# Optimization experiments

Measured on AMD Instinct MI355X. Metric: run time of the kernel, lower is better.

## Reference

```python
import jax, jax.numpy as jnp
import numpy as np

EMBED_DIM = 32
PIC_RES = 96
KERNEL_BW = 3.0
STEP_SIZE = 0.5
NB_ITERS = 3


def setup_inputs() -> dict:
    key = jax.random.key(0)
    # scale down so exp(bw * x^T x) stays in a safe numeric range
    x_in = jax.random.normal(key, (1, EMBED_DIM, PIC_RES, PIC_RES), dtype=jnp.float32) * 0.1
    return {"x_in": x_in}


def reference(x_in):
    # x: [D, N], N = res*res pixels
    x = x_in.reshape(EMBED_DIM, -1)
    outs = []
    for _ in range(NB_ITERS):
        # affinity K[i,j] = exp(bw * <x_i, x_j>), shape [N, N]
        K = jnp.exp(KERNEL_BW * (x.T @ x))
        # column sums d_j = sum_i K[i,j] (== torch diag(K^T @ 1)); K is symmetric
        d = K.sum(axis=0)
        # x <- x @ (step * K diag(1/d) + (1-step) I)
        x = STEP_SIZE * (x @ K) / d + (1.0 - STEP_SIZE) * x
        outs.append(x.reshape(EMBED_DIM, PIC_RES, PIC_RES))
    final = x.reshape(EMBED_DIM, PIC_RES, PIC_RES)
    return final, jnp.stack(outs)
```

## Files before the change

### kernel.cpp

```cpp
#include <hip/hip_runtime.h>
#include <hip/hip_bf16.h>
#include <math.h>


#define D 32
#define NPIX 9216
#define NSPLIT 16
#define JB 256
#define NJB (NPIX / JB)
#define IPB (NPIX / NSPLIT)
#define ICH 64
#define XST 56
#define TS  40

typedef __attribute__((ext_vector_type(8))) short short8;
typedef __attribute__((ext_vector_type(4))) short short4v;
typedef __attribute__((ext_vector_type(4))) float f32x4;

#if __has_builtin(__builtin_amdgcn_exp2f)
#define EXP2F __builtin_amdgcn_exp2f
#else
#define EXP2F exp2f
#endif

#define C3 4.32808512266689f

__device__ __forceinline__ unsigned pack2_bf16(float a, float b) {
    union { __hip_bfloat162 h2; unsigned u; } c;
    c.h2 = __float22bfloat162_rn(make_float2(a, b));
    return c.u;
}
__device__ __forceinline__ short pack1_bf16(float a) {
    union { __hip_bfloat16 h; unsigned short s; } c;
    c.h = __float2bfloat16(a);
    return (short)c.s;
}

__global__ __launch_bounds__(256, 2) void accum_kernel(
    const short* __restrict__ xb,
    const short* __restrict__ xbT,
    float* __restrict__ num_part,
    float* __restrict__ den_part)
{
    __shared__ __align__(16) short xiT_s[2][32 * XST];
    __shared__ __align__(16) short xi_s [2][32 * XST];

    const int t = threadIdx.x;
    const int wid = t >> 6, lane = t & 63, quad = lane >> 4, m = lane & 15;
    const int bj = blockIdx.x % NJB, bi = blockIdx.x / NJB;
    const int j0 = bj * JB + wid * 64;
    const int i0b = bi * IPB;

    short8 bfrag[4];
#pragma unroll
    for (int jt = 0; jt < 4; ++jt)
        bfrag[jt] = *(const short8*)&xbT[(size_t)(j0 + jt * 16 + m) * D + quad * 8];

    f32x4 acc[2][4] = {};
    float dacc[4] = {0.f, 0.f, 0.f, 0.f};

    const int srT = t >> 2, hT = srT >> 5, ilT = srT & 31, cT = (t & 3) * 8;
    const int sgm = ((ilT & 4) << 2) + ((ilT >> 3) << 2) + (ilT & 3);
    const int dV = t >> 3, cV = (t & 7) >> 2, qV = (t & 3) * 8;

    for (int ic = 0; ic < IPB; ic += ICH) {
        const int i0 = i0b + ic;
        __syncthreads();
        *(short8*)&xiT_s[hT][sgm * XST + cT] =
            *(const short8*)&xbT[(size_t)(i0 + srT) * D + cT];
        *(short8*)&xi_s[cV][dV * XST + qV] =
            *(const short8*)&xb[dV * NPIX + i0 + cV * 32 + qV];
        __syncthreads();

#pragma unroll
        for (int h = 0; h < 2; ++h) {
            short8 aT0 = *(const short8*)&xiT_s[h][m * XST + quad * 8];
            short8 aT1 = *(const short8*)&xiT_s[h][(16 + m) * XST + quad * 8];
            short8 aV0 = *(const short8*)&xi_s[h][m * XST + quad * 8];
            short8 aV1 = *(const short8*)&xi_s[h][(16 + m) * XST + quad * 8];

#pragma unroll
            for (int jt = 0; jt < 4; ++jt) {
                f32x4 z = {0.f, 0.f, 0.f, 0.f};
                f32x4 s0 = __builtin_amdgcn_mfma_f32_16x16x32_bf16(aT0, bfrag[jt], z, 0, 0, 0);
                f32x4 s1 = __builtin_amdgcn_mfma_f32_16x16x32_bf16(aT1, bfrag[jt], z, 0, 0, 0);

                float w[8];
#pragma unroll
                for (int r = 0; r < 4; ++r) { w[r]     = EXP2F(C3 * s0[r]);
                                              w[4 + r] = EXP2F(C3 * s1[r]); }
#pragma unroll
                for (int r = 0; r < 8; ++r) dacc[jt] += w[r];

                union { short8 s; unsigned u[4]; } wb;
                wb.u[0] = pack2_bf16(w[0], w[1]);
                wb.u[1] = pack2_bf16(w[2], w[3]);
                wb.u[2] = pack2_bf16(w[4], w[5]);
                wb.u[3] = pack2_bf16(w[6], w[7]);

                acc[0][jt] = __builtin_amdgcn_mfma_f32_16x16x32_bf16(aV0, wb.s, acc[0][jt], 0, 0, 0);
                acc[1][jt] = __builtin_amdgcn_mfma_f32_16x16x32_bf16(aV1, wb.s, acc[1][jt], 0, 0, 0);
            }
        }
    }

    float* np = num_part + (size_t)bi * D * NPIX;
#pragma unroll
    for (int dt = 0; dt < 2; ++dt)
#pragma unroll
        for (int jt = 0; jt < 4; ++jt)
#pragma unroll
            for (int r = 0; r < 4; ++r)
                np[(dt * 16 + quad * 4 + r) * NPIX + j0 + jt * 16 + m] = acc[dt][jt][r];
#pragma unroll
    for (int jt = 0; jt < 4; ++jt) {
        float v = dacc[jt];
        v += __shfl_xor(v, 16, 64);
        v += __shfl_xor(v, 32, 64);
        if (quad == 0) den_part[bi * NPIX + j0 + jt * 16 + m] = v;
    }
}

__global__ __launch_bounds__(256) void combine_kernel(
    const float* __restrict__ xin,
    const float* __restrict__ num_part, const float* __restrict__ den_part,
    float* __restrict__ xout, float* __restrict__ xfinal,
    short* __restrict__ xb, short* __restrict__ xbT, int do_ms)
{
    __shared__ __align__(16) short tile[32 * TS];
    const int t = threadIdx.x;
    const int il = t & 31, q = t >> 5;
    const int i = blockIdx.x * 32 + il;
    const int d0 = q * 4;

    float inv = 0.f;
    if (do_ms) {
        float den = 0.f;
#pragma unroll
        for (int s = 0; s < NSPLIT; ++s) den += den_part[s * NPIX + i];
        inv = 0.5f / den;
    }

#pragma unroll
    for (int dd = 0; dd < 4; ++dd) {
        const int d = d0 + dd;
        const int idx = d * NPIX + i;
        float v;
        if (do_ms) {
            float nm = 0.f;
#pragma unroll
            for (int s = 0; s < NSPLIT; ++s) nm += num_part[(s * D + d) * NPIX + i];
            v = nm * inv + 0.5f * xin[idx];
            xout[idx] = v;
            if (xfinal) xfinal[idx] = v;
        } else {
            v = xin[idx];
        }
        short b = pack1_bf16(v);
        xb[idx] = b;
        tile[il * TS + d] = b;
    }
    __syncthreads();
    const int i2 = t >> 3, dc = (t & 7) * 4;
    *(short4v*)&xbT[(blockIdx.x * 32 + i2) * D + dc] =
        *(const short4v*)&tile[i2 * TS + dc];
}

extern "C" void kernel_launch(void* const* d_in, const int* in_sizes, int n_in,
                              void* d_out, int out_size, void* d_ws, size_t ws_size,
                              hipStream_t stream)
{
    const float* x0 = (const float*)d_in[0];
    float* out = (float*)d_out;
    const size_t slot = (size_t)D * NPIX;

    float* num_part = (float*)d_ws;
    float* den_part = num_part + (size_t)NSPLIT * slot;
    short* xb  = (short*)(den_part + (size_t)NSPLIT * NPIX);
    short* xbT = xb + slot;

    combine_kernel<<<dim3(NPIX / 32), dim3(256), 0, stream>>>(
        x0, nullptr, nullptr, nullptr, nullptr, xb, xbT, 0);

    for (int t = 0; t < 3; ++t) {
        accum_kernel<<<dim3(NJB * NSPLIT), dim3(256), 0, stream>>>(
            xb, xbT, num_part, den_part);
        const float* xin = (t == 0) ? x0 : (out + (size_t)t * slot);
        combine_kernel<<<dim3(NPIX / 32), dim3(256), 0, stream>>>(
            xin, num_part, den_part, out + (size_t)(t + 1) * slot,
            (t == 2) ? out : nullptr, xb, xbT, 1);
    }
}
```

Baseline: 173.2 us.

## Accumulate split-K partials with atomics and shrink accum blocks to 128 threads

Replaces the per-split partial numerator and denominator buffers with float atomicAdd into a single accumulator. The combine kernel reads that accumulator directly and zeroes it for the next iteration. The accum kernel now uses 128-thread blocks covering 128 columns, with each thread loading two LDS tiles, which doubles the grid size and targets higher occupancy. This removes the 16-way partial write and readback traffic, at the cost of atomic contention and a floating-point summation order that is no longer deterministic.

```diff
diff --git a/kernel.cpp b/kernel.cpp
--- a/kernel.cpp
+++ b/kernel.cpp
@@ -6,7 +6,7 @@
 #define D 32
 #define NPIX 9216
 #define NSPLIT 16
-#define JB 256
+#define JB 128
 #define NJB (NPIX / JB)
 #define IPB (NPIX / NSPLIT)
 #define ICH 64
@@ -36,11 +36,11 @@
     return (short)c.s;
 }
 
-__global__ __launch_bounds__(256, 2) void accum_kernel(
+__global__ __launch_bounds__(128, 4) void accum_kernel(
     const short* __restrict__ xb,
     const short* __restrict__ xbT,
-    float* __restrict__ num_part,
-    float* __restrict__ den_part)
+    float* __restrict__ num,
+    float* __restrict__ den)
 {
     __shared__ __align__(16) short xiT_s[2][32 * XST];
     __shared__ __align__(16) short xi_s [2][32 * XST];
@@ -59,17 +59,19 @@
     f32x4 acc[2][4] = {};
     float dacc[4] = {0.f, 0.f, 0.f, 0.f};
 
-    const int srT = t >> 2, hT = srT >> 5, ilT = srT & 31, cT = (t & 3) * 8;
-    const int sgm = ((ilT & 4) << 2) + ((ilT >> 3) << 2) + (ilT & 3);
-    const int dV = t >> 3, cV = (t & 7) >> 2, qV = (t & 3) * 8;
+    const int srow = t >> 2, scol = (t & 3) * 8;
+    const int sgm = ((srow & 4) << 2) + ((srow >> 3) << 2) + (srow & 3);
 
     for (int ic = 0; ic < IPB; ic += ICH) {
         const int i0 = i0b + ic;
         __syncthreads();
-        *(short8*)&xiT_s[hT][sgm * XST + cT] =
-            *(const short8*)&xbT[(size_t)(i0 + srT) * D + cT];
-        *(short8*)&xi_s[cV][dV * XST + qV] =
-            *(const short8*)&xb[dV * NPIX + i0 + cV * 32 + qV];
+#pragma unroll
+        for (int k = 0; k < 2; ++k) {
+            *(short8*)&xiT_s[k][sgm * XST + scol] =
+                *(const short8*)&xbT[(size_t)(i0 + k * 32 + srow) * D + scol];
+            *(short8*)&xi_s[k][srow * XST + scol] =
+                *(const short8*)&xb[srow * NPIX + i0 + k * 32 + scol];
+        }
         __syncthreads();
 
 #pragma unroll
@@ -89,8 +91,9 @@
 #pragma unroll
                 for (int r = 0; r < 4; ++r) { w[r]     = EXP2F(C3 * s0[r]);
                                               w[4 + r] = EXP2F(C3 * s1[r]); }
-#pragma unroll
-                for (int r = 0; r < 8; ++r) dacc[jt] += w[r];
+                float p0 = (w[0] + w[1]) + (w[2] + w[3]);
+                float p1 = (w[4] + w[5]) + (w[6] + w[7]);
+                dacc[jt] += p0 + p1;
 
                 union { short8 s; unsigned u[4]; } wb;
                 wb.u[0] = pack2_bf16(w[0], w[1]);
@@ -104,26 +107,26 @@
         }
     }
 
-    float* np = num_part + (size_t)bi * D * NPIX;
 #pragma unroll
     for (int dt = 0; dt < 2; ++dt)
 #pragma unroll
         for (int jt = 0; jt < 4; ++jt)
 #pragma unroll
             for (int r = 0; r < 4; ++r)
-                np[(dt * 16 + quad * 4 + r) * NPIX + j0 + jt * 16 + m] = acc[dt][jt][r];
+                atomicAdd(&num[(dt * 16 + quad * 4 + r) * NPIX + j0 + jt * 16 + m],
+                          acc[dt][jt][r]);
 #pragma unroll
     for (int jt = 0; jt < 4; ++jt) {
         float v = dacc[jt];
         v += __shfl_xor(v, 16, 64);
         v += __shfl_xor(v, 32, 64);
-        if (quad == 0) den_part[bi * NPIX + j0 + jt * 16 + m] = v;
+        if (quad == 0) atomicAdd(&den[j0 + jt * 16 + m], v);
     }
 }
 
 __global__ __launch_bounds__(256) void combine_kernel(
     const float* __restrict__ xin,
-    const float* __restrict__ num_part, const float* __restrict__ den_part,
+    float* __restrict__ num, float* __restrict__ den,
     float* __restrict__ xout, float* __restrict__ xfinal,
     short* __restrict__ xb, short* __restrict__ xbT, int do_ms)
 {
@@ -134,12 +137,7 @@
     const int d0 = q * 4;
 
     float inv = 0.f;
-    if (do_ms) {
-        float den = 0.f;
-#pragma unroll
-        for (int s = 0; s < NSPLIT; ++s) den += den_part[s * NPIX + i];
-        inv = 0.5f / den;
-    }
+    if (do_ms) inv = 0.5f / den[i];
 
 #pragma unroll
     for (int dd = 0; dd < 4; ++dd) {
@@ -147,22 +145,21 @@
         const int idx = d * NPIX + i;
         float v;
         if (do_ms) {
-            float nm = 0.f;
-#pragma unroll
-            for (int s = 0; s < NSPLIT; ++s) nm += num_part[(s * D + d) * NPIX + i];
-            v = nm * inv + 0.5f * xin[idx];
+            v = num[idx] * inv + 0.5f * xin[idx];
             xout[idx] = v;
             if (xfinal) xfinal[idx] = v;
         } else {
             v = xin[idx];
         }
+        num[idx] = 0.f;
         short b = pack1_bf16(v);
         xb[idx] = b;
         tile[il * TS + d] = b;
     }
     __syncthreads();
+    if (t < 32) den[blockIdx.x * 32 + t] = 0.f;
     const int i2 = t >> 3, dc = (t & 7) * 4;
-    *(short4v*)&xbT[(blockIdx.x * 32 + i2) * D + dc] =
+    *(short4v*)&xbT[(size_t)(blockIdx.x * 32 + i2) * D + dc] =
         *(const short4v*)&tile[i2 * TS + dc];
 }
 
@@ -174,20 +171,19 @@
     float* out = (float*)d_out;
     const size_t slot = (size_t)D * NPIX;
 
-    float* num_part = (float*)d_ws;
-    float* den_part = num_part + (size_t)NSPLIT * slot;
-    short* xb  = (short*)(den_part + (size_t)NSPLIT * NPIX);
+    float* num = (float*)d_ws;
+    float* den = num + slot;
+    short* xb  = (short*)(den + NPIX);
     short* xbT = xb + slot;
 
     combine_kernel<<<dim3(NPIX / 32), dim3(256), 0, stream>>>(
-        x0, nullptr, nullptr, nullptr, nullptr, xb, xbT, 0);
+        x0, num, den, nullptr, nullptr, xb, xbT, 0);
 
     for (int t = 0; t < 3; ++t) {
-        accum_kernel<<<dim3(NJB * NSPLIT), dim3(256), 0, stream>>>(
-            xb, xbT, num_part, den_part);
+        accum_kernel<<<dim3(NJB * NSPLIT), dim3(128), 0, stream>>>(xb, xbT, num, den);
         const float* xin = (t == 0) ? x0 : (out + (size_t)t * slot);
         combine_kernel<<<dim3(NPIX / 32), dim3(256), 0, stream>>>(
-            xin, num_part, den_part, out + (size_t)(t + 1) * slot,
+            xin, num, den, out + (size_t)(t + 1) * slot,
             (t == 2) ? out : nullptr, xb, xbT, 1);
     }
 }
```

New measurement: 190.0 us. 1.1x slower.
